# Kernel tuning notes

Measured on AMD Instinct MI355X. Metric: run time of the kernel, lower is better.

Reference implementation:

```python
import jax, jax.numpy as jnp
import numpy as np

N, T = 64, 256
TOTAL_NODES, C_IN = 25, 128          # c = 3200
NUM_SEEDS, C_OUT = 5, 3              # seeds flat dim = 15
NEW_NODES = 20
LIN_IN = TOTAL_NODES * C_IN + NUM_SEEDS * C_OUT  # 3215


def setup_inputs() -> dict:
    key = jax.random.key(0)
    k1, k2, k3 = jax.random.split(key, 3)
    x = jax.random.normal(k1, (N, T, TOTAL_NODES * C_IN), dtype=jnp.float32)
    seeds = jax.random.normal(k2, (N, T, NUM_SEEDS, C_OUT), dtype=jnp.float32)
    # Stacked weights of the `new_nodes` cloned Linear(LIN_IN, C_OUT) layers.
    W = jax.random.normal(k3, (NEW_NODES, C_OUT, LIN_IN), dtype=jnp.float32) * 0.02
    b = jnp.zeros((NEW_NODES, C_OUT), dtype=jnp.float32)
    return {"x": x, "seeds": seeds, "W": W, "b": b}


def reference(x, seeds, W, b):
    n, t, _ = x.shape
    mix = jnp.concatenate([x, seeds.reshape(n, t, -1)], axis=2)  # [n,t,LIN_IN]
    # Fuse all cloned small Linears into one batched GEMM, then layout as
    # torch.stack([...], dim=3): output [n, t, c_out, new_nodes].
    out = jnp.einsum('ntc,koc->ntok', mix, W) + b.T  # b.T: [c_out, new_nodes]
    return out
```

## Files before the change

kernel.cpp:

```cpp
#include <hip/hip_runtime.h>


#define NROWS    16384
#define CIN      3200
#define SEED_K   15
#define LIN_IN   3215
#define NCOL     60
#define KB_MAIN  100
#define KB_TOT   101
#define WB_ELEMS (KB_TOT * 4 * 64 * 8)

typedef __attribute__((ext_vector_type(8))) __bf16 bf16x8;
typedef __attribute__((ext_vector_type(4))) float f32x4;
typedef __attribute__((ext_vector_type(8))) unsigned short ushort8;

__device__ inline unsigned short f2bf_rne(float f) {
    unsigned int u = __builtin_bit_cast(unsigned int, f);
    u += 0x7fffu + ((u >> 16) & 1u);
    return (unsigned short)(u >> 16);
}

__device__ inline bf16x8 to_bf16x8(f32x4 a0, f32x4 a1) {
    ushort8 u;
    u[0] = f2bf_rne(a0[0]); u[1] = f2bf_rne(a0[1]);
    u[2] = f2bf_rne(a0[2]); u[3] = f2bf_rne(a0[3]);
    u[4] = f2bf_rne(a1[0]); u[5] = f2bf_rne(a1[1]);
    u[6] = f2bf_rne(a1[2]); u[7] = f2bf_rne(a1[3]);
    return __builtin_bit_cast(bf16x8, u);
}

__global__ void prep_B(const float* __restrict__ W, unsigned short* __restrict__ Wb) {
    int idx = blockIdx.x * blockDim.x + threadIdx.x;
    if (idx >= WB_ELEMS) return;
    int jj   = idx & 7;
    int lane = (idx >> 3) & 63;
    int nt   = (idx >> 9) & 3;
    int kb   = idx >> 11;
    int k = kb * 32 + (lane >> 4) * 8 + jj;
    int n = nt * 16 + (lane & 15);
    float v = 0.0f;
    if (k < LIN_IN && n < NCOL) {
        int o = n / 20, kn = n % 20;
        v = W[(kn * 3 + o) * LIN_IN + k];
    }
    Wb[idx] = f2bf_rne(v);
}

__global__ __launch_bounds__(256) void gen_nodes_gemm(
    const float* __restrict__ x, const float* __restrict__ seeds,
    const float* __restrict__ b, const unsigned short* __restrict__ Wb,
    float* __restrict__ out) {
    const int lane = threadIdx.x & 63;
    const int wave = threadIdx.x >> 6;
    const int quad = lane >> 4;
    const int l15  = lane & 15;
    const int row_base = blockIdx.x * 64 + wave * 16;
    const int arow = row_base + l15;

    const float* xrow = x + (size_t)arow * CIN + quad * 8;

    f32x4 acc[4];
#pragma unroll
    for (int i = 0; i < 4; ++i) acc[i] = (f32x4){0.f, 0.f, 0.f, 0.f};

#pragma unroll 4
    for (int kb = 0; kb < KB_MAIN; ++kb) {
        const f32x4* ap = (const f32x4*)(xrow + kb * 32);
        f32x4 a0 = ap[0];
        f32x4 a1 = ap[1];
        const unsigned short* bb = Wb + (size_t)kb * 2048 + lane * 8;
        bf16x8 b0 = *(const bf16x8*)(bb);
        bf16x8 b1 = *(const bf16x8*)(bb + 512);
        bf16x8 b2 = *(const bf16x8*)(bb + 1024);
        bf16x8 b3 = *(const bf16x8*)(bb + 1536);
        bf16x8 af = to_bf16x8(a0, a1);
        acc[0] = __builtin_amdgcn_mfma_f32_16x16x32_bf16(af, b0, acc[0], 0, 0, 0);
        acc[1] = __builtin_amdgcn_mfma_f32_16x16x32_bf16(af, b1, acc[1], 0, 0, 0);
        acc[2] = __builtin_amdgcn_mfma_f32_16x16x32_bf16(af, b2, acc[2], 0, 0, 0);
        acc[3] = __builtin_amdgcn_mfma_f32_16x16x32_bf16(af, b3, acc[3], 0, 0, 0);
    }

    {
        const float* srow = seeds + (size_t)arow * SEED_K;
        f32x4 s0 = {0.f, 0.f, 0.f, 0.f}, s1 = {0.f, 0.f, 0.f, 0.f};
#pragma unroll
        for (int j = 0; j < 4; ++j) {
            int c = quad * 8 + j;
            if (c < SEED_K) s0[j] = srow[c];
            if (c + 4 < SEED_K) s1[j] = srow[c + 4];
        }
        bf16x8 af = to_bf16x8(s0, s1);
        const unsigned short* bb = Wb + (size_t)KB_MAIN * 2048 + lane * 8;
        bf16x8 b0 = *(const bf16x8*)(bb);
        bf16x8 b1 = *(const bf16x8*)(bb + 512);
        bf16x8 b2 = *(const bf16x8*)(bb + 1024);
        bf16x8 b3 = *(const bf16x8*)(bb + 1536);
        acc[0] = __builtin_amdgcn_mfma_f32_16x16x32_bf16(af, b0, acc[0], 0, 0, 0);
        acc[1] = __builtin_amdgcn_mfma_f32_16x16x32_bf16(af, b1, acc[1], 0, 0, 0);
        acc[2] = __builtin_amdgcn_mfma_f32_16x16x32_bf16(af, b2, acc[2], 0, 0, 0);
        acc[3] = __builtin_amdgcn_mfma_f32_16x16x32_bf16(af, b3, acc[3], 0, 0, 0);
    }

#pragma unroll
    for (int nt = 0; nt < 4; ++nt) {
        int j = nt * 16 + l15;
        if (j < NCOL) {
            float bias = b[(j % 20) * 3 + (j / 20)];
#pragma unroll
            for (int r = 0; r < 4; ++r) {
                int m = quad * 4 + r;
                out[(size_t)(row_base + m) * NCOL + j] = acc[nt][r] + bias;
            }
        }
    }
}

extern "C" void kernel_launch(void* const* d_in, const int* in_sizes, int n_in,
                              void* d_out, int out_size, void* d_ws, size_t ws_size,
                              hipStream_t stream) {
    const float* x     = (const float*)d_in[0];
    const float* seeds = (const float*)d_in[1];
    const float* W     = (const float*)d_in[2];
    const float* b     = (const float*)d_in[3];
    float* out = (float*)d_out;
    unsigned short* Wb = (unsigned short*)d_ws;

    prep_B<<<(WB_ELEMS + 255) / 256, 256, 0, stream>>>(W, Wb);
    gen_nodes_gemm<<<NROWS / 64, 256, 0, stream>>>(x, seeds, b, Wb, out);
}
```

Baseline: 308.7 us.

## Split K dimension across blocks with separate partial-sum reduction kernel

The GEMM is split into four K-slices so the grid grows from 256 to 1024 blocks, giving more waves to hide memory latency on a part with many CUs. Each block writes fp32 partial results to workspace, and a new reduction kernel sums the slices and adds the bias. This adds a kernel launch and extra partial-sum traffic, roughly 16 MB written and read, in exchange for higher occupancy when streaming the ~210 MB input.

```diff
diff --git a/kernel.cpp b/kernel.cpp
--- a/kernel.cpp
+++ b/kernel.cpp
@@ -9,6 +9,9 @@
 #define KB_MAIN  100
 #define KB_TOT   101
 #define WB_ELEMS (KB_TOT * 4 * 64 * 8)
+#define NSPLIT   4
+#define KB_PER_SPLIT 25
+#define PART_OFF 524288
 
 typedef __attribute__((ext_vector_type(8))) __bf16 bf16x8;
 typedef __attribute__((ext_vector_type(4))) float f32x4;
@@ -48,27 +51,29 @@
 
 __global__ __launch_bounds__(256) void gen_nodes_gemm(
     const float* __restrict__ x, const float* __restrict__ seeds,
-    const float* __restrict__ b, const unsigned short* __restrict__ Wb,
-    float* __restrict__ out) {
+    const unsigned short* __restrict__ Wb, float* __restrict__ part) {
     const int lane = threadIdx.x & 63;
     const int wave = threadIdx.x >> 6;
     const int quad = lane >> 4;
     const int l15  = lane & 15;
-    const int row_base = blockIdx.x * 64 + wave * 16;
+    const int split = blockIdx.x >> 8;
+    const int row_base = (blockIdx.x & 255) * 64 + wave * 16;
     const int arow = row_base + l15;
 
-    const float* xrow = x + (size_t)arow * CIN + quad * 8;
+    const int kb0 = split * KB_PER_SPLIT;
+    const float* xrow = x + (size_t)arow * CIN + quad * 8 + kb0 * 32;
+    const unsigned short* wb0 = Wb + (size_t)kb0 * 2048 + lane * 8;
 
     f32x4 acc[4];
 #pragma unroll
     for (int i = 0; i < 4; ++i) acc[i] = (f32x4){0.f, 0.f, 0.f, 0.f};
 
-#pragma unroll 4
-    for (int kb = 0; kb < KB_MAIN; ++kb) {
+#pragma unroll 5
+    for (int kb = 0; kb < KB_PER_SPLIT; ++kb) {
         const f32x4* ap = (const f32x4*)(xrow + kb * 32);
         f32x4 a0 = ap[0];
         f32x4 a1 = ap[1];
-        const unsigned short* bb = Wb + (size_t)kb * 2048 + lane * 8;
+        const unsigned short* bb = wb0 + (size_t)kb * 2048;
         bf16x8 b0 = *(const bf16x8*)(bb);
         bf16x8 b1 = *(const bf16x8*)(bb + 512);
         bf16x8 b2 = *(const bf16x8*)(bb + 1024);
@@ -80,7 +85,7 @@
         acc[3] = __builtin_amdgcn_mfma_f32_16x16x32_bf16(af, b3, acc[3], 0, 0, 0);
     }
 
-    {
+    if (split == NSPLIT - 1) {
         const float* srow = seeds + (size_t)arow * SEED_K;
         f32x4 s0 = {0.f, 0.f, 0.f, 0.f}, s1 = {0.f, 0.f, 0.f, 0.f};
 #pragma unroll
@@ -101,18 +106,28 @@
         acc[3] = __builtin_amdgcn_mfma_f32_16x16x32_bf16(af, b3, acc[3], 0, 0, 0);
     }
 
+    float* pw = part + ((size_t)split * NROWS + row_base) * 64;
 #pragma unroll
     for (int nt = 0; nt < 4; ++nt) {
-        int j = nt * 16 + l15;
-        if (j < NCOL) {
-            float bias = b[(j % 20) * 3 + (j / 20)];
 #pragma unroll
-            for (int r = 0; r < 4; ++r) {
-                int m = quad * 4 + r;
-                out[(size_t)(row_base + m) * NCOL + j] = acc[nt][r] + bias;
-            }
+        for (int r = 0; r < 4; ++r) {
+            pw[(size_t)(quad * 4 + r) * 64 + nt * 16 + l15] = acc[nt][r];
         }
     }
+}
+
+__global__ __launch_bounds__(256) void reduce_out(
+    const float* __restrict__ part, const float* __restrict__ b,
+    float* __restrict__ out) {
+    int idx = blockIdx.x * blockDim.x + threadIdx.x;
+    int c = idx & 63;
+    int m = idx >> 6;
+    if (c >= NCOL) return;
+    float s = b[(c % 20) * 3 + (c / 20)];
+#pragma unroll
+    for (int sp = 0; sp < NSPLIT; ++sp)
+        s += part[((size_t)sp * NROWS + m) * 64 + c];
+    out[(size_t)m * NCOL + c] = s;
 }
 
 extern "C" void kernel_launch(void* const* d_in, const int* in_sizes, int n_in,
@@ -124,7 +139,9 @@
     const float* b     = (const float*)d_in[3];
     float* out = (float*)d_out;
     unsigned short* Wb = (unsigned short*)d_ws;
+    float* part = (float*)((char*)d_ws + PART_OFF);
 
     prep_B<<<(WB_ELEMS + 255) / 256, 256, 0, stream>>>(W, Wb);
-    gen_nodes_gemm<<<NROWS / 64, 256, 0, stream>>>(x, seeds, b, Wb, out);
+    gen_nodes_gemm<<<NSPLIT * 256, 256, 0, stream>>>(x, seeds, Wb, part);
+    reduce_out<<<NROWS * 64 / 256, 256, 0, stream>>>(part, b, out);
 }
```

After: 309.4 us. Within noise of the previous version (+0.2%).

## Split output column tiles across wave pairs to double block count

Applied to the files above, without the earlier changes.

Each 16-row tile is now handled by a pair of waves, each computing two of the four 16-column output tiles, so a block covers 32 rows and the grid doubles to 512 blocks. This raises parallelism and memory-level concurrency for the bandwidth-bound read of x (about 210 MB). The cost is that each x row is loaded and converted to bf16 twice, once per wave of the pair, which leans on L2/L1 for reuse.

```diff
diff --git a/kernel.cpp b/kernel.cpp
--- a/kernel.cpp
+++ b/kernel.cpp
@@ -52,32 +52,30 @@
     float* __restrict__ out) {
     const int lane = threadIdx.x & 63;
     const int wave = threadIdx.x >> 6;
+    const int pair = wave >> 1;
+    const int half = wave & 1;
     const int quad = lane >> 4;
     const int l15  = lane & 15;
-    const int row_base = blockIdx.x * 64 + wave * 16;
+    const int row_base = blockIdx.x * 32 + pair * 16;
     const int arow = row_base + l15;
 
     const float* xrow = x + (size_t)arow * CIN + quad * 8;
+    const unsigned short* wb0 = Wb + half * 1024 + lane * 8;
 
-    f32x4 acc[4];
-#pragma unroll
-    for (int i = 0; i < 4; ++i) acc[i] = (f32x4){0.f, 0.f, 0.f, 0.f};
+    f32x4 acc0 = {0.f, 0.f, 0.f, 0.f};
+    f32x4 acc1 = {0.f, 0.f, 0.f, 0.f};
 
 #pragma unroll 4
     for (int kb = 0; kb < KB_MAIN; ++kb) {
         const f32x4* ap = (const f32x4*)(xrow + kb * 32);
         f32x4 a0 = ap[0];
         f32x4 a1 = ap[1];
-        const unsigned short* bb = Wb + (size_t)kb * 2048 + lane * 8;
+        const unsigned short* bb = wb0 + (size_t)kb * 2048;
         bf16x8 b0 = *(const bf16x8*)(bb);
         bf16x8 b1 = *(const bf16x8*)(bb + 512);
-        bf16x8 b2 = *(const bf16x8*)(bb + 1024);
-        bf16x8 b3 = *(const bf16x8*)(bb + 1536);
         bf16x8 af = to_bf16x8(a0, a1);
-        acc[0] = __builtin_amdgcn_mfma_f32_16x16x32_bf16(af, b0, acc[0], 0, 0, 0);
-        acc[1] = __builtin_amdgcn_mfma_f32_16x16x32_bf16(af, b1, acc[1], 0, 0, 0);
-        acc[2] = __builtin_amdgcn_mfma_f32_16x16x32_bf16(af, b2, acc[2], 0, 0, 0);
-        acc[3] = __builtin_amdgcn_mfma_f32_16x16x32_bf16(af, b3, acc[3], 0, 0, 0);
+        acc0 = __builtin_amdgcn_mfma_f32_16x16x32_bf16(af, b0, acc0, 0, 0, 0);
+        acc1 = __builtin_amdgcn_mfma_f32_16x16x32_bf16(af, b1, acc1, 0, 0, 0);
     }
 
     {
@@ -90,26 +88,23 @@
             if (c + 4 < SEED_K) s1[j] = srow[c + 4];
         }
         bf16x8 af = to_bf16x8(s0, s1);
-        const unsigned short* bb = Wb + (size_t)KB_MAIN * 2048 + lane * 8;
+        const unsigned short* bb = Wb + (size_t)KB_MAIN * 2048 + half * 1024 + lane * 8;
         bf16x8 b0 = *(const bf16x8*)(bb);
         bf16x8 b1 = *(const bf16x8*)(bb + 512);
-        bf16x8 b2 = *(const bf16x8*)(bb + 1024);
-        bf16x8 b3 = *(const bf16x8*)(bb + 1536);
-        acc[0] = __builtin_amdgcn_mfma_f32_16x16x32_bf16(af, b0, acc[0], 0, 0, 0);
-        acc[1] = __builtin_amdgcn_mfma_f32_16x16x32_bf16(af, b1, acc[1], 0, 0, 0);
-        acc[2] = __builtin_amdgcn_mfma_f32_16x16x32_bf16(af, b2, acc[2], 0, 0, 0);
-        acc[3] = __builtin_amdgcn_mfma_f32_16x16x32_bf16(af, b3, acc[3], 0, 0, 0);
+        acc0 = __builtin_amdgcn_mfma_f32_16x16x32_bf16(af, b0, acc0, 0, 0, 0);
+        acc1 = __builtin_amdgcn_mfma_f32_16x16x32_bf16(af, b1, acc1, 0, 0, 0);
     }
 
 #pragma unroll
-    for (int nt = 0; nt < 4; ++nt) {
-        int j = nt * 16 + l15;
+    for (int nt2 = 0; nt2 < 2; ++nt2) {
+        const f32x4 acc = nt2 ? acc1 : acc0;
+        int j = (half * 2 + nt2) * 16 + l15;
         if (j < NCOL) {
             float bias = b[(j % 20) * 3 + (j / 20)];
 #pragma unroll
             for (int r = 0; r < 4; ++r) {
                 int m = quad * 4 + r;
-                out[(size_t)(row_base + m) * NCOL + j] = acc[nt][r] + bias;
+                out[(size_t)(row_base + m) * NCOL + j] = acc[r] + bias;
             }
         }
     }
@@ -126,5 +121,5 @@
     unsigned short* Wb = (unsigned short*)d_ws;
 
     prep_B<<<(WB_ELEMS + 255) / 256, 256, 0, stream>>>(W, Wb);
-    gen_nodes_gemm<<<NROWS / 64, 256, 0, stream>>>(x, seeds, b, Wb, out);
+    gen_nodes_gemm<<<NROWS / 32, 256, 0, stream>>>(x, seeds, b, Wb, out);
 }
```

Result: no change. 309.7 us (+0.3%).
